# Optimization experiments

Hardware: AMD Instinct MI355X
Metric: run time of the kernel (lower is better)

Reference implementation:

```python
import jax, jax.numpy as jnp
import numpy as np

K = 1024      # size_codebook
D = 64        # dim_codebook
N = 131072    # number of input vectors
GAMMA = 0.99
ALPHA = 1e-09
BETA = 0.25


def setup_inputs() -> dict:
    key = jax.random.key(0)
    k1, k2, k3 = jax.random.split(key, 3)
    X = jax.random.normal(k1, (N, D), dtype=jnp.float32)
    E = jax.random.normal(k2, (K, D), dtype=jnp.float32)
    cluster_sizes = jnp.zeros((K,), dtype=jnp.float32)
    moving_avg = E  # buffer initialized to a clone of E.weight
    return {"X": X, "E": E, "cluster_sizes": cluster_sizes, "moving_avg": moving_avg}


def reference(X, E, cluster_sizes, moving_avg):
    # squared euclidean distances: [N, K]
    X_sqnorm = jnp.sum(X * X, axis=1, keepdims=True)          # [N, 1]
    E_sqnorm = jnp.sum(E * E, axis=1)[None, :]                # [1, K]
    dist = X_sqnorm + E_sqnorm - 2.0 * (X @ E.T)              # [N, K]
    min_dist = jnp.min(dist, axis=1)                          # [N]
    argmins = jnp.argmin(dist, axis=1)                        # [N]
    Z_embs_raw = E[argmins]                                   # [N, D]

    # commitment loss (codebook is detached in the EMA variant)
    diff = X - jax.lax.stop_gradient(Z_embs_raw)
    loss = BETA * jnp.mean(jnp.sum(diff * diff, axis=1))

    # EMA codebook update (training mode, no-grad in torch)
    counts = jax.ops.segment_sum(jnp.ones((N,), dtype=X.dtype), argmins, num_segments=K)
    cs = GAMMA * cluster_sizes + (1.0 - GAMMA) * counts
    cs = (cs + ALPHA) / (1.0 + ALPHA * K / jnp.sum(cs))
    sums = jax.ops.segment_sum(X, argmins, num_segments=K)    # one_hot.T @ X, [K, D]
    ma = GAMMA * moving_avg + (1.0 - GAMMA) * sums
    E_new = ma / cs[:, None]

    # straight-through estimator
    Z_embs = X + jax.lax.stop_gradient(Z_embs_raw - X)
    return (Z_embs, loss, argmins, min_dist, E_new, cs, ma)
```

## Files before the change

### kernel.cpp

```cpp
#include <hip/hip_runtime.h>
#include <math.h>

#define NN 131072
#define KK 1024
#define DD 64
#define GAMMA 0.99f
#define ALPHA 1e-9f
#define BETA 0.25f

typedef float f32x4 __attribute__((ext_vector_type(4)));
typedef short bf16x8 __attribute__((ext_vector_type(8)));

__device__ __constant__ float OMG = (float)(1.0 - 0.99);

__device__ __forceinline__ void split_bf16(float v, unsigned short& h, unsigned short& l) {
    unsigned int b = __float_as_uint(v);
    unsigned int hb = b & 0xFFFF0000u;
    h = (unsigned short)(hb >> 16);
    float r = v - __uint_as_float(hb);
    unsigned int lb = __float_as_uint(r);
    lb += 0x7FFFu + ((lb >> 16) & 1u);
    l = (unsigned short)(lb >> 16);
}

__global__ __launch_bounds__(64)
void vq_prep(const float* __restrict__ E, float4* __restrict__ Efrag,
             float* __restrict__ esq) {
    int nt = blockIdx.x;
    int l = threadIdx.x;
    int n = nt * 16 + (l & 15);
    int kb = (l >> 4) * 8;
    float ss = 0.f;
    #pragma unroll
    for (int ks = 0; ks < 2; ++ks) {
        const float4* xp = (const float4*)(E + (size_t)n * DD + ks * 32 + kb);
        float4 a = xp[0], b = xp[1];
        float v[8] = {a.x, a.y, a.z, a.w, b.x, b.y, b.z, b.w};
        union { float4 f; unsigned short u[8]; } H, L;
        #pragma unroll
        for (int j = 0; j < 8; ++j) {
            unsigned short hh, ll;
            split_bf16(v[j], hh, ll);
            H.u[j] = hh; L.u[j] = ll;
            ss = fmaf(v[j], v[j], ss);
        }
        int fid = nt * 4 + ks * 2;
        Efrag[(size_t)(fid + 0) * 64 + l] = H.f;
        Efrag[(size_t)(fid + 1) * 64 + l] = L.f;
    }
    ss += __shfl_xor(ss, 16, 64);
    ss += __shfl_xor(ss, 32, 64);
    if (l < 16) esq[nt * 16 + l] = ss;
}

#define BM 128

__global__ __launch_bounds__(256, 2)
void vq_main(const float* __restrict__ X, const float* __restrict__ E,
             const float4* __restrict__ Efrag, const float* __restrict__ esq,
             float* __restrict__ argf, float* __restrict__ mind,
             float* __restrict__ Z, float* __restrict__ counts,
             float* __restrict__ sums, float* __restrict__ loss_part) {
    __shared__ float redv[256];
    __shared__ int redi[256];
    __shared__ int bidx[128];

    int tid = threadIdx.x;
    int lane = tid & 63, w = tid >> 6;
    int rg = w & 1, cg = w >> 1;
    int lc = lane & 15, lq = lane >> 4;

    size_t R0 = (size_t)blockIdx.x * BM + rg * 64;

    bf16x8 ah[4][2], al[4][2];
    #pragma unroll
    for (int mt = 0; mt < 4; ++mt) {
        #pragma unroll
        for (int ks = 0; ks < 2; ++ks) {
            const float4* xp =
                (const float4*)(X + (R0 + mt * 16 + lc) * DD + ks * 32 + lq * 8);
            float4 x0 = xp[0], x1 = xp[1];
            float v[8] = {x0.x, x0.y, x0.z, x0.w, x1.x, x1.y, x1.z, x1.w};
            union { bf16x8 s; unsigned short u[8]; } H, L;
            #pragma unroll
            for (int j = 0; j < 8; ++j) {
                unsigned short hh, ll;
                split_bf16(v[j], hh, ll);
                H.u[j] = hh; L.u[j] = ll;
            }
            ah[mt][ks] = H.s;
            al[mt][ks] = L.s;
        }
    }

    float bestv[4][4];
    int besti[4][4];
    #pragma unroll
    for (int mt = 0; mt < 4; ++mt)
        #pragma unroll
        for (int r = 0; r < 4; ++r) { bestv[mt][r] = 3.402823466e38f; besti[mt][r] = 0; }

    const float4* bp = Efrag + (size_t)(cg * 32) * 256 + lane;
    const float* ep = esq + cg * 512 + lc;

    float4 nb0 = bp[0], nb1 = bp[64], nb2 = bp[128], nb3 = bp[192];
    float en = ep[0];

    for (int nt = 0; nt < 32; ++nt) {
        float4 cb0 = nb0, cb1 = nb1, cb2 = nb2, cb3 = nb3;
        float ec = en;
        if (nt < 31) {
            const float4* q = bp + (size_t)(nt + 1) * 256;
            nb0 = q[0]; nb1 = q[64]; nb2 = q[128]; nb3 = q[192];
            en = ep[(nt + 1) * 16];
        }
        union { float4 f; bf16x8 s; } u0, u1, u2, u3;
        u0.f = cb0; u1.f = cb1; u2.f = cb2; u3.f = cb3;
        bf16x8 bh0 = u0.s, bl0 = u1.s, bh1 = u2.s, bl1 = u3.s;

        f32x4 acc[4];
        #pragma unroll
        for (int mt = 0; mt < 4; ++mt) acc[mt] = (f32x4){0.f, 0.f, 0.f, 0.f};

        #pragma unroll
        for (int mt = 0; mt < 4; ++mt)
            acc[mt] = __builtin_amdgcn_mfma_f32_16x16x32_bf16(ah[mt][0], bh0, acc[mt], 0, 0, 0);
        #pragma unroll
        for (int mt = 0; mt < 4; ++mt)
            acc[mt] = __builtin_amdgcn_mfma_f32_16x16x32_bf16(ah[mt][1], bh1, acc[mt], 0, 0, 0);
        #pragma unroll
        for (int mt = 0; mt < 4; ++mt)
            acc[mt] = __builtin_amdgcn_mfma_f32_16x16x32_bf16(ah[mt][0], bl0, acc[mt], 0, 0, 0);
        #pragma unroll
        for (int mt = 0; mt < 4; ++mt)
            acc[mt] = __builtin_amdgcn_mfma_f32_16x16x32_bf16(ah[mt][1], bl1, acc[mt], 0, 0, 0);
        #pragma unroll
        for (int mt = 0; mt < 4; ++mt)
            acc[mt] = __builtin_amdgcn_mfma_f32_16x16x32_bf16(al[mt][0], bh0, acc[mt], 0, 0, 0);
        #pragma unroll
        for (int mt = 0; mt < 4; ++mt)
            acc[mt] = __builtin_amdgcn_mfma_f32_16x16x32_bf16(al[mt][1], bh1, acc[mt], 0, 0, 0);

        int n = cg * 512 + nt * 16 + lc;
        #pragma unroll
        for (int mt = 0; mt < 4; ++mt) {
            #pragma unroll
            for (int r = 0; r < 4; ++r) {
                float sc = fmaf(-2.f, acc[mt][r], ec);
                if (sc < bestv[mt][r]) { bestv[mt][r] = sc; besti[mt][r] = n; }
            }
        }
    }

    #pragma unroll
    for (int off = 1; off <= 8; off <<= 1) {
        #pragma unroll
        for (int mt = 0; mt < 4; ++mt) {
            #pragma unroll
            for (int r = 0; r < 4; ++r) {
                float ov = __shfl_xor(bestv[mt][r], off, 64);
                int oi = __shfl_xor(besti[mt][r], off, 64);
                if (ov < bestv[mt][r] || (ov == bestv[mt][r] && oi < besti[mt][r])) {
                    bestv[mt][r] = ov; besti[mt][r] = oi;
                }
            }
        }
    }
    if (lc == 0) {
        #pragma unroll
        for (int mt = 0; mt < 4; ++mt)
            #pragma unroll
            for (int r = 0; r < 4; ++r) {
                int row = rg * 64 + mt * 16 + lq * 4 + r;
                redv[row * 2 + cg] = bestv[mt][r];
                redi[row * 2 + cg] = besti[mt][r];
            }
    }
    __syncthreads();
    if (tid < 128) {
        float v0 = redv[tid * 2], v1 = redv[tid * 2 + 1];
        int i0 = redi[tid * 2], i1 = redi[tid * 2 + 1];
        bidx[tid] = (v1 < v0 || (v1 == v0 && i1 < i0)) ? i1 : i0;
    }
    __syncthreads();

    float lsum = 0.f;
    for (int it = 0; it < 32; ++it) {
        int row = w * 32 + it;
        int bi = bidx[row];
        size_t grow = (size_t)blockIdx.x * BM + row;
        float x = X[grow * DD + lane];
        float e = E[(size_t)bi * DD + lane];
        Z[grow * DD + lane] = x + (e - x);
        float d = x - e;
        float s = d * d;
        #pragma unroll
        for (int m = 32; m; m >>= 1) s += __shfl_xor(s, m, 64);
        atomicAdd(&sums[bi * DD + lane], x);
        if (lane == 0) {
            atomicAdd(&counts[bi], 1.0f);
            argf[grow] = (float)bi;
            mind[grow] = s;
        }
        lsum += s;
    }
    if (lane == 0) atomicAdd(&loss_part[(blockIdx.x * 4 + w) & 1023], lsum);
}

__global__ __launch_bounds__(1024)
void vq_cs(const float* __restrict__ cluster_sizes, const float* __restrict__ counts,
           const float* __restrict__ loss_part, float* __restrict__ out_cs,
           float* __restrict__ out_loss) {
    __shared__ float red[1024];
    int k = threadIdx.x;
    float csr = GAMMA * cluster_sizes[k] + OMG * counts[k];
    red[k] = csr;
    __syncthreads();
    for (int off = 512; off; off >>= 1) {
        if (k < off) red[k] += red[k + off];
        __syncthreads();
    }
    float total = red[0];
    __syncthreads();
    red[k] = loss_part[k];
    __syncthreads();
    for (int off = 512; off; off >>= 1) {
        if (k < off) red[k] += red[k + off];
        __syncthreads();
    }
    if (k == 0) out_loss[0] = BETA * (red[0] / (float)NN);

    float denom = 1.0f + (ALPHA * (float)KK) / total;
    out_cs[k] = (csr + ALPHA) / denom;
}

__global__ __launch_bounds__(256)
void vq_ema(const float* __restrict__ moving_avg, const float* __restrict__ sums,
            const float* __restrict__ cs, float* __restrict__ out_ma,
            float* __restrict__ out_enew) {
    int idx = blockIdx.x * 256 + threadIdx.x;
    int k = idx >> 6;
    float ma = GAMMA * moving_avg[idx] + OMG * sums[idx];
    out_ma[idx] = ma;
    out_enew[idx] = ma / cs[k];
}

extern "C" void kernel_launch(void* const* d_in, const int* in_sizes, int n_in,
                              void* d_out, int out_size, void* d_ws, size_t ws_size,
                              hipStream_t stream) {
    const float* X = (const float*)d_in[0];
    const float* E = (const float*)d_in[1];
    const float* cluster_sizes = (const float*)d_in[2];
    const float* moving_avg = (const float*)d_in[3];

    float* out = (float*)d_out;
    float* o_Z = out;
    float* o_loss = o_Z + (size_t)NN * DD;
    float* o_arg = o_loss + 1;
    float* o_mind = o_arg + NN;
    float* o_enew = o_mind + NN;
    float* o_cs = o_enew + (size_t)KK * DD;
    float* o_ma = o_cs + KK;

    float* ws = (float*)d_ws;
    float* counts = ws;
    float* sums = counts + KK;
    float* loss_part = sums + (size_t)KK * DD;
    float* esq = loss_part + 1024;
    float4* Efrag = (float4*)(esq + KK);

    hipMemsetAsync(d_ws, 0, (KK + (size_t)KK * DD + 1024) * sizeof(float), stream);

    vq_prep<<<KK / 16, 64, 0, stream>>>(E, Efrag, esq);
    vq_main<<<NN / BM, 256, 0, stream>>>(X, E, Efrag, esq, o_arg, o_mind, o_Z,
                                         counts, sums, loss_part);
    vq_cs<<<1, 1024, 0, stream>>>(cluster_sizes, counts, loss_part, o_cs, o_loss);
    vq_ema<<<(KK * DD) / 256, 256, 0, stream>>>(moving_avg, sums, o_cs, o_ma, o_enew);
}
```

Measured before the change: 231.0 us.

## Replace per-element sum atomics with per-code row lists and gather kernel

Instead of having every row atomically add 64 floats into the cluster sums, the main kernel appends the row index to a per-code bucket (capped by workspace size). A new kernel gathers each code's rows and computes the sums together with the EMA outputs. Rows that overflow the cap fall back to float atomics. It also raises launch bounds occupancy to 4 and adds unroll pragmas. The aim is to cut atomic contention on hot codes, at the cost of a second pass over X and possible load imbalance across codes.

```diff
diff --git a/kernel.cpp b/kernel.cpp
--- a/kernel.cpp
+++ b/kernel.cpp
@@ -55,12 +55,13 @@
 
 #define BM 128
 
-__global__ __launch_bounds__(256, 2)
+__global__ __launch_bounds__(256, 4)
 void vq_main(const float* __restrict__ X, const float* __restrict__ E,
              const float4* __restrict__ Efrag, const float* __restrict__ esq,
              float* __restrict__ argf, float* __restrict__ mind,
-             float* __restrict__ Z, float* __restrict__ counts,
-             float* __restrict__ sums, float* __restrict__ loss_part) {
+             float* __restrict__ Z, int* __restrict__ cursor,
+             int* __restrict__ rowlist, float* __restrict__ sumsFB,
+             float* __restrict__ loss_part, int cap) {
     __shared__ float redv[256];
     __shared__ int redi[256];
     __shared__ int bidx[128];
@@ -106,6 +107,7 @@
     float4 nb0 = bp[0], nb1 = bp[64], nb2 = bp[128], nb3 = bp[192];
     float en = ep[0];
 
+    #pragma unroll 2
     for (int nt = 0; nt < 32; ++nt) {
         float4 cb0 = nb0, cb1 = nb1, cb2 = nb2, cb3 = nb3;
         float ec = en;
@@ -185,6 +187,7 @@
     __syncthreads();
 
     float lsum = 0.f;
+    #pragma unroll 4
     for (int it = 0; it < 32; ++it) {
         int row = w * 32 + it;
         int bi = bidx[row];
@@ -196,24 +199,30 @@
         float s = d * d;
         #pragma unroll
         for (int m = 32; m; m >>= 1) s += __shfl_xor(s, m, 64);
-        atomicAdd(&sums[bi * DD + lane], x);
+        int pos = 0;
         if (lane == 0) {
-            atomicAdd(&counts[bi], 1.0f);
+            pos = atomicAdd(&cursor[bi], 1);
             argf[grow] = (float)bi;
             mind[grow] = s;
         }
+        pos = __shfl(pos, 0, 64);
+        if (pos < cap) {
+            if (lane == 0) rowlist[(size_t)bi * cap + pos] = (int)grow;
+        } else {
+            atomicAdd(&sumsFB[(size_t)bi * DD + lane], x);
+        }
         lsum += s;
     }
     if (lane == 0) atomicAdd(&loss_part[(blockIdx.x * 4 + w) & 1023], lsum);
 }
 
 __global__ __launch_bounds__(1024)
-void vq_cs(const float* __restrict__ cluster_sizes, const float* __restrict__ counts,
+void vq_cs(const float* __restrict__ cluster_sizes, const int* __restrict__ cursor,
            const float* __restrict__ loss_part, float* __restrict__ out_cs,
            float* __restrict__ out_loss) {
     __shared__ float red[1024];
     int k = threadIdx.x;
-    float csr = GAMMA * cluster_sizes[k] + OMG * counts[k];
+    float csr = GAMMA * cluster_sizes[k] + OMG * (float)cursor[k];
     red[k] = csr;
     __syncthreads();
     for (int off = 512; off; off >>= 1) {
@@ -235,14 +244,31 @@
 }
 
 __global__ __launch_bounds__(256)
-void vq_ema(const float* __restrict__ moving_avg, const float* __restrict__ sums,
-            const float* __restrict__ cs, float* __restrict__ out_ma,
-            float* __restrict__ out_enew) {
-    int idx = blockIdx.x * 256 + threadIdx.x;
-    int k = idx >> 6;
-    float ma = GAMMA * moving_avg[idx] + OMG * sums[idx];
-    out_ma[idx] = ma;
-    out_enew[idx] = ma / cs[k];
+void vq_sum_ema(const float* __restrict__ X, const int* __restrict__ rowlist,
+                const int* __restrict__ cursor, const float* __restrict__ sumsFB,
+                const float* __restrict__ cs, const float* __restrict__ mavg,
+                float* __restrict__ o_ma, float* __restrict__ o_enew, int cap) {
+    __shared__ float part[4][64];
+    int k = blockIdx.x;
+    int lane = threadIdx.x & 63, w = threadIdx.x >> 6;
+    int cnt = cursor[k];
+    int nr = cnt < cap ? cnt : cap;
+    const int* rl = rowlist + (size_t)k * cap;
+    float acc = 0.f;
+    #pragma unroll 2
+    for (int i = w; i < nr; i += 4) {
+        int r = rl[i];
+        acc += X[(size_t)r * DD + lane];
+    }
+    part[w][lane] = acc;
+    __syncthreads();
+    if (w == 0) {
+        float s = part[0][lane] + part[1][lane] + part[2][lane] + part[3][lane]
+                + sumsFB[(size_t)k * DD + lane];
+        float ma = GAMMA * mavg[(size_t)k * DD + lane] + OMG * s;
+        o_ma[(size_t)k * DD + lane] = ma;
+        o_enew[(size_t)k * DD + lane] = ma / cs[k];
+    }
 }
 
 extern "C" void kernel_launch(void* const* d_in, const int* in_sizes, int n_in,
@@ -262,18 +288,23 @@
     float* o_cs = o_enew + (size_t)KK * DD;
     float* o_ma = o_cs + KK;
 
-    float* ws = (float*)d_ws;
-    float* counts = ws;
-    float* sums = counts + KK;
-    float* loss_part = sums + (size_t)KK * DD;
-    float* esq = loss_part + 1024;
+    int* cursor = (int*)d_ws;
+    float* loss_part = (float*)d_ws + 1024;
+    float* sumsFB = loss_part + 1024;
+    float* esq = sumsFB + (size_t)KK * DD;
     float4* Efrag = (float4*)(esq + KK);
-
-    hipMemsetAsync(d_ws, 0, (KK + (size_t)KK * DD + 1024) * sizeof(float), stream);
+    int* rowlist = (int*)(esq + KK + (size_t)KK * DD);
+
+    size_t base_bytes = (size_t)(1024 + 1024 + KK * DD + KK + KK * DD) * 4;
+    long cap_l = ((long)ws_size - (long)base_bytes) / (long)(KK * sizeof(int));
+    int cap = cap_l < 0 ? 0 : (cap_l > 1024 ? 1024 : (int)cap_l);
+
+    hipMemsetAsync(d_ws, 0, (size_t)(1024 + 1024 + KK * DD) * 4, stream);
 
     vq_prep<<<KK / 16, 64, 0, stream>>>(E, Efrag, esq);
     vq_main<<<NN / BM, 256, 0, stream>>>(X, E, Efrag, esq, o_arg, o_mind, o_Z,
-                                         counts, sums, loss_part);
-    vq_cs<<<1, 1024, 0, stream>>>(cluster_sizes, counts, loss_part, o_cs, o_loss);
-    vq_ema<<<(KK * DD) / 256, 256, 0, stream>>>(moving_avg, sums, o_cs, o_ma, o_enew);
-}
+                                         cursor, rowlist, sumsFB, loss_part, cap);
+    vq_cs<<<1, 1024, 0, stream>>>(cluster_sizes, cursor, loss_part, o_cs, o_loss);
+    vq_sum_ema<<<KK, 256, 0, stream>>>(X, rowlist, cursor, sumsFB, o_cs,
+                                       moving_avg, o_ma, o_enew, cap);
+}
```

Measured after the change: 399.9 us. 1.73x slower.
